# Performance work log

Hardware: AMD Instinct MI355X
Metric: run time of the kernel (lower is better)

## Reference

```python
import jax, jax.numpy as jnp
import numpy as np

N, D, E = 50000, 128, 800000
BN_EPS = 1e-5


def _gcn(x, W, b, row, col, val):
    # dropout with p=0.0 is identity; h = x @ W; out = adj @ h + b (COO SpMM)
    h = x @ W                                    # [N, d]
    msg = val[:, None] * h[col]                  # [E, d] gather + scale
    agg = jax.ops.segment_sum(msg, row, num_segments=x.shape[0])  # scatter-add
    return agg + b


def _predictor(x, W1, b1, gamma, beta, a, W2, b2):
    h = x @ W1 + b1
    mu = jnp.mean(h, axis=0)
    var = jnp.mean((h - mu) ** 2, axis=0)        # biased var (torch BN train mode)
    hn = (h - mu) / jnp.sqrt(var + BN_EPS) * gamma + beta
    hp = jnp.where(hn >= 0, hn, a * hn)          # PReLU, single shared alpha
    return hp @ W2 + b2


def _byol_loss(p, t):
    pn = p / jnp.linalg.norm(p, axis=-1, keepdims=True)
    tn = t / jnp.linalg.norm(t, axis=-1, keepdims=True)
    return 2.0 - 2.0 * jnp.sum(pn * tn, axis=-1)


def setup_inputs() -> dict:
    key = jax.random.key(0)
    ks = jax.random.split(key, 16)
    xavier = float(np.sqrt(6.0 / (D + D)))
    x = jax.random.normal(ks[0], (N, D), dtype=jnp.float32)
    perb = 0.05 * jax.random.normal(ks[1], (N, D), dtype=jnp.float32)
    edge_row = jax.random.randint(ks[2], (E,), 0, N, dtype=jnp.int32)
    edge_col = jax.random.randint(ks[3], (E,), 0, N, dtype=jnp.int32)
    edge_val = jax.random.uniform(ks[4], (E,), dtype=jnp.float32)
    W = jax.random.uniform(ks[5], (D, D), minval=-xavier, maxval=xavier, dtype=jnp.float32)
    b = jnp.zeros((D,), dtype=jnp.float32)
    # target encoder is a deepcopy at init; give it its own values to test the math
    Wt = jax.random.uniform(ks[6], (D, D), minval=-xavier, maxval=xavier, dtype=jnp.float32)
    bt = jnp.zeros((D,), dtype=jnp.float32)
    lin = float(1.0 / np.sqrt(D))
    W1 = jax.random.uniform(ks[7], (D, D), minval=-lin, maxval=lin, dtype=jnp.float32)
    b1 = jax.random.uniform(ks[8], (D,), minval=-lin, maxval=lin, dtype=jnp.float32)
    bn_gamma = jnp.ones((D,), dtype=jnp.float32)
    bn_beta = jnp.zeros((D,), dtype=jnp.float32)
    prelu_a = jnp.asarray(0.25, dtype=jnp.float32)
    W2 = jax.random.uniform(ks[9], (D, D), minval=-lin, maxval=lin, dtype=jnp.float32)
    b2 = jax.random.uniform(ks[10], (D,), minval=-lin, maxval=lin, dtype=jnp.float32)
    return dict(x=x, perb=perb, edge_row=edge_row, edge_col=edge_col, edge_val=edge_val,
                W=W, b=b, Wt=Wt, bt=bt, W1=W1, b1=b1, bn_gamma=bn_gamma,
                bn_beta=bn_beta, prelu_a=prelu_a, W2=W2, b2=b2)


def reference(x, perb, edge_row, edge_col, edge_val, W, b, Wt, bt,
              W1, b1, bn_gamma, bn_beta, prelu_a, W2, b2):
    x1 = x
    x2 = x + perb
    enc_x2 = _gcn(x2, W, b, edge_row, edge_col, edge_val)
    embed = x2 + enc_x2
    online_x = _gcn(x1, W, b, edge_row, edge_col, edge_val)
    online_y = enc_x2
    target_y = jax.lax.stop_gradient(_gcn(x1, Wt, bt, edge_row, edge_col, edge_val))
    target_x = jax.lax.stop_gradient(_gcn(x2, Wt, bt, edge_row, edge_col, edge_val))
    px = _predictor(online_x, W1, b1, bn_gamma, bn_beta, prelu_a, W2, b2)
    py = _predictor(online_y, W1, b1, bn_gamma, bn_beta, prelu_a, W2, b2)
    loss = jnp.mean(_byol_loss(px, target_x) + _byol_loss(py, target_y))
    return embed, loss
```

## Files before the change

### kernel.cpp

```cpp
#include <hip/hip_runtime.h>
#include <hip/hip_fp16.h>
#include <stdint.h>

typedef unsigned short u16;
typedef unsigned int u32;
typedef unsigned char u8;
typedef __attribute__((ext_vector_type(8))) short bf16x8;
typedef __attribute__((ext_vector_type(4))) short bf16x4;
typedef __attribute__((ext_vector_type(4))) float f32x4;

#define DD 128
#define CAP 64
#define STRA 136
#define STRCF 132
#define PSC 256.f
#define IPSC (1.f/256.f)

__device__ __forceinline__ float bflo(u32 u){ return __uint_as_float(u<<16); }
__device__ __forceinline__ float bfhi(u32 u){ return __uint_as_float(u & 0xffff0000u); }
__device__ __forceinline__ float bf2f(u16 u){ return __uint_as_float(((u32)u)<<16); }
__device__ __forceinline__ u16 f2bf(float f){
  u32 u = __float_as_uint(f);
  return (u16)((u + 0x7fffu + ((u>>16)&1u)) >> 16);
}

#define FMAXP(g, vv, vqv) do { \
    ax[0] += (vv)*bflo((g).x); ax[1] += (vv)*bfhi((g).x); \
    ax[2] += (vv)*bflo((g).y); ax[3] += (vv)*bfhi((g).y); \
    int d_ = (int)(g).z; \
    ap[0] += (vqv)*(float)(signed char)(d_); \
    ap[1] += (vqv)*(float)(signed char)(d_>>8); \
    ap[2] += (vqv)*(float)(signed char)(d_>>16); \
    ap[3] += (vqv)*(float)(d_>>24); } while(0)

__global__ __launch_bounds__(256) void kU_init(
    const float* __restrict__ x, const float* __restrict__ perb,
    const float* __restrict__ W, const float* __restrict__ Wt,
    const float* __restrict__ W1, const float* __restrict__ W2,
    u8* __restrict__ Tg, u16* __restrict__ Bswz,
    u16* __restrict__ W1swz, u16* __restrict__ W2swz,
    int* __restrict__ deg, float* __restrict__ stats,
    float* __restrict__ gbuf, int N)
{
  int f = blockIdx.x*256 + threadIdx.x;
  if (f < N) deg[f] = 0;
  if (f < 512) stats[f] = 0.f;
  if (f < 64) gbuf[f] = 0.f;
  if (f < 65536) {
    int idx = f;
    if (idx < 32768) {
      int j = idx & 7, lane = (idx>>3)&63, nt = (idx>>9)&15, kt = idx>>13;
      int k = kt*32 + (lane>>4)*8 + j, n = nt*16 + (lane&15);
      float v = (n < DD) ? W[k*DD + n] : Wt[k*DD + (n-DD)];
      Bswz[idx] = f2bf(v);
    } else {
      int t = idx - 32768;
      int which = t >> 14; t &= 16383;
      int j = t & 7, lane = (t>>3)&63, nt = (t>>9)&7, kt = (t>>12)&3;
      int k = kt*32 + (lane>>4)*8 + j, n = nt*16 + (lane&15);
      const float* __restrict__ src = which ? W2 : W1;
      u16* __restrict__ dst = which ? W2swz : W1swz;
      dst[t] = f2bf(src[k*DD + n]);
    }
  }
  if (f < N*32) {
    int r = f >> 5, hl = f & 31;
    float4 xa = *(const float4*)(x    + (size_t)r*DD + hl*4);
    float4 pa = *(const float4*)(perb + (size_t)r*DD + hl*4);
    u32 d0 = (u32)f2bf(xa.x) | ((u32)f2bf(xa.y) << 16);
    u32 d1 = (u32)f2bf(xa.z) | ((u32)f2bf(xa.w) << 16);
    int q0 = (int)rintf(pa.x*PSC); q0 = q0 < -127 ? -127 : (q0 > 127 ? 127 : q0);
    int q1 = (int)rintf(pa.y*PSC); q1 = q1 < -127 ? -127 : (q1 > 127 ? 127 : q1);
    int q2 = (int)rintf(pa.z*PSC); q2 = q2 < -127 ? -127 : (q2 > 127 ? 127 : q2);
    int q3 = (int)rintf(pa.w*PSC); q3 = q3 < -127 ? -127 : (q3 > 127 ? 127 : q3);
    u32 d2 = (u32)(q0 & 0xff) | ((u32)(q1 & 0xff) << 8)
           | ((u32)(q2 & 0xff) << 16) | ((u32)(q3 & 0xff) << 24);
    uint3 o; o.x = d0; o.y = d1; o.z = d2;
    *(uint3*)(Tg + (size_t)r*384 + hl*12) = o;
  }
}

__global__ __launch_bounds__(256) void k2_bucket(
    const int* __restrict__ row, const int* __restrict__ col,
    const float* __restrict__ val, int E, int* __restrict__ deg,
    u32* __restrict__ perm, int* __restrict__ ovfc, int* __restrict__ ovf)
{
  int e = blockIdx.x*256 + threadIdx.x;
  if (e >= E) return;
  int r = row[e];
  int slot = atomicAdd(&deg[r], 1);
  if (slot < CAP) {
    u32 pk = (u32)(col[e] & 0xffff)
           | ((u32)__half_as_ushort(__float2half(val[e])) << 16);
    perm[(size_t)r*CAP + slot] = pk;
  }
  else { int oi = atomicAdd(ovfc, 1); if (oi < 4096) ovf[oi] = e; }
}

__global__ __launch_bounds__(256) void k3_spmm(
    const u32* __restrict__ perm, const int* __restrict__ deg,
    const u8* __restrict__ Tg, u16* __restrict__ T2, int N)
{
  int row = blockIdx.x*4 + (threadIdx.x >> 6);
  int l = threadIdx.x & 63;
  if (row >= N) return;
  int dg = deg[row];
  dg = dg < 0 ? 0 : (dg > CAP ? CAP : dg);
  const int half = l >> 5, hl = l & 31;
  const int loff = hl * 12;
  float ax[4] = {0.f,0.f,0.f,0.f};
  float ap[4] = {0.f,0.f,0.f,0.f};
  for (int base = 0; base < dg; base += 64) {
    u32 pk = 0;
    if (base + l < dg) pk = perm[(size_t)row*CAP + base + l];
    int mm = dg - base; if (mm > 64) mm = 64;
    int kmax = (mm + 1) & ~1;
    int j = 0;
    for (; j + 8 <= kmax; j += 8) {
      u32 p0 = (u32)__shfl((int)pk, j + half);
      u32 p1 = (u32)__shfl((int)pk, j + 2 + half);
      u32 p2 = (u32)__shfl((int)pk, j + 4 + half);
      u32 p3 = (u32)__shfl((int)pk, j + 6 + half);
      int c0 = p0 & 0xffff; c0 = (c0 < N) ? c0 : 0;
      int c1 = p1 & 0xffff; c1 = (c1 < N) ? c1 : 0;
      int c2 = p2 & 0xffff; c2 = (c2 < N) ? c2 : 0;
      int c3 = p3 & 0xffff; c3 = (c3 < N) ? c3 : 0;
      float v0 = __half2float(__ushort_as_half((u16)(p0 >> 16)));
      float v1 = __half2float(__ushort_as_half((u16)(p1 >> 16)));
      float v2 = __half2float(__ushort_as_half((u16)(p2 >> 16)));
      float v3 = __half2float(__ushort_as_half((u16)(p3 >> 16)));
      uint3 g0 = *(const uint3*)(Tg + (size_t)c0*384 + loff);
      uint3 g1 = *(const uint3*)(Tg + (size_t)c1*384 + loff);
      uint3 g2 = *(const uint3*)(Tg + (size_t)c2*384 + loff);
      uint3 g3 = *(const uint3*)(Tg + (size_t)c3*384 + loff);
      float vq0 = v0*IPSC, vq1 = v1*IPSC, vq2 = v2*IPSC, vq3 = v3*IPSC;
      FMAXP(g0, v0, vq0); FMAXP(g1, v1, vq1);
      FMAXP(g2, v2, vq2); FMAXP(g3, v3, vq3);
    }
    for (; j < kmax; j += 2) {
      u32 p0 = (u32)__shfl((int)pk, j + half);
      int c0 = p0 & 0xffff; c0 = (c0 < N) ? c0 : 0;
      float v0 = __half2float(__ushort_as_half((u16)(p0 >> 16)));
      uint3 g0 = *(const uint3*)(Tg + (size_t)c0*384 + loff);
      float vq0 = v0*IPSC;
      FMAXP(g0, v0, vq0);
    }
  }
  #pragma unroll
  for (int i = 0; i < 4; ++i) {
    ax[i] += __shfl_xor(ax[i], 32);
    ap[i] += __shfl_xor(ap[i], 32);
  }
  bf16x4 ob;
  #pragma unroll
  for (int i = 0; i < 4; ++i) {
    float o = half ? (ax[i] + ap[i]) : ax[i];
    ob[i] = (short)f2bf(o);
  }
  *(bf16x4*)(T2 + (size_t)row*256 + half*128 + hl*4) = ob;
}

__global__ __launch_bounds__(256) void k3b_ovf(
    const int* __restrict__ rowI, const int* __restrict__ colI,
    const float* __restrict__ val, const int* __restrict__ ovfc,
    const int* __restrict__ ovf, const u8* __restrict__ Tg,
    u16* __restrict__ T2)
{
  int n = *ovfc; if (n > 4096) n = 4096;
  for (int i = 0; i < n; ++i) {
    int e = ovf[i];
    int r = rowI[e], c = colI[e];
    float v = val[e];
    int d = threadIdx.x;
    int dl = d & 127;
    const u8* tgc = Tg + (size_t)c*384 + (dl>>2)*12;
    float xv = bf2f(*(const u16*)(tgc + (dl&3)*2));
    float add = v * xv;
    if (d >= 128) {
      int qb = (int)(signed char)tgc[8 + (dl&3)];
      add = v * (xv + (float)qb * IPSC);
    }
    u16* p = &T2[(size_t)r*256 + d];
    *p = f2bf(bf2f(*p) + add);
  }
}

__global__ __launch_bounds__(256, 4) void k4_gemm(
    const u16* __restrict__ T2, const u16* __restrict__ Bswz,
    const u16* __restrict__ W1swz,
    const float* __restrict__ b, const float* __restrict__ bt,
    const float* __restrict__ b1, const u8* __restrict__ Tg,
    u16* __restrict__ AGGb, float* __restrict__ outE,
    u16* __restrict__ Px, u16* __restrict__ Py,
    float* __restrict__ partial, int N, int NB)
{
  __shared__ __align__(16) u16 As1[64*STRA];
  __shared__ __align__(16) u16 Ct[64*STRA];
  const int tid = threadIdx.x;
  const int r0 = blockIdx.x * 32;
  #pragma unroll
  for (int i = 0; i < 4; ++i) {
    int f = tid + 256*i;
    int row = f >> 4, c8 = f & 15;
    int r = r0 + (row & 31);
    bf16x8 ch = {0,0,0,0,0,0,0,0};
    if (r < N) ch = *(const bf16x8*)(T2 + (size_t)r*256 + (row>>5)*128 + c8*8);
    *(bf16x8*)&As1[row*STRA + c8*8] = ch;
  }
  __syncthreads();
  const int w = tid >> 6, l = tid & 63;
  const int m = l & 15, q = l >> 4;
  const int arow = w*16 + m;
  f32x4 acc[8];
  #pragma unroll
  for (int nt = 0; nt < 8; ++nt) acc[nt] = (f32x4){0.f,0.f,0.f,0.f};
  #pragma unroll
  for (int kt = 0; kt < 4; ++kt) {
    bf16x8 af = *(const bf16x8*)&As1[arow*STRA + kt*32 + q*8];
    #pragma unroll
    for (int nt = 0; nt < 8; ++nt) {
      bf16x8 bfr = *(const bf16x8*)(Bswz + ((size_t)(kt*16 + 8 + nt)*64 + l)*8);
      acc[nt] = __builtin_amdgcn_mfma_f32_16x16x32_bf16(af, bfr, acc[nt], 0, 0, 0);
    }
  }
  #pragma unroll
  for (int nt = 0; nt < 8; ++nt) {
    float bv = bt[nt*16 + m];
    #pragma unroll
    for (int i = 0; i < 4; ++i)
      Ct[(w*16 + q*4 + i)*STRA + nt*16 + m] = f2bf(acc[nt][i] + bv);
  }
  __syncthreads();
  {
    const int ar = tid >> 2, p = tid & 3;
    const int src = r0 + (ar & 31);
    if (src < N) {
      u16* dp = AGGb + (size_t)src*256 + (ar>>5)*128 + p*32;
      const u16* sp = &Ct[ar*STRA + p*32];
      #pragma unroll
      for (int i = 0; i < 4; ++i)
        *(bf16x8*)(dp + i*8) = *(const bf16x8*)(sp + i*8);
    }
  }
  __syncthreads();
  #pragma unroll
  for (int nt = 0; nt < 8; ++nt) acc[nt] = (f32x4){0.f,0.f,0.f,0.f};
  #pragma unroll
  for (int kt = 0; kt < 4; ++kt) {
    bf16x8 af = *(const bf16x8*)&As1[arow*STRA + kt*32 + q*8];
    #pragma unroll
    for (int nt = 0; nt < 8; ++nt) {
      bf16x8 bfr = *(const bf16x8*)(Bswz + ((size_t)(kt*16 + nt)*64 + l)*8);
      acc[nt] = __builtin_amdgcn_mfma_f32_16x16x32_bf16(af, bfr, acc[nt], 0, 0, 0);
    }
  }
  #pragma unroll
  for (int nt = 0; nt < 8; ++nt) {
    float bv = b[nt*16 + m];
    #pragma unroll
    for (int i = 0; i < 4; ++i)
      Ct[(w*16 + q*4 + i)*STRA + nt*16 + m] = f2bf(acc[nt][i] + bv);
  }
  __syncthreads();
  #pragma unroll
  for (int i = 0; i < 2; ++i) {
    int f = tid + 256*i;
    int rr = f >> 4, c8 = f & 15;
    int src = r0 + rr;
    if (src < N) {
      const u16* cp = &Ct[(32+rr)*STRA + c8*8];
      const u8* tg = Tg + (size_t)src*384 + c8*24;
      uint3 ga = *(const uint3*)tg;
      uint3 gb = *(const uint3*)(tg + 12);
      int da = (int)ga.z, db = (int)gb.z;
      float4 e0, e1;
      e0.x = bflo(ga.x) + IPSC*(float)(signed char)(da)     + bf2f(cp[0]);
      e0.y = bfhi(ga.x) + IPSC*(float)(signed char)(da>>8)  + bf2f(cp[1]);
      e0.z = bflo(ga.y) + IPSC*(float)(signed char)(da>>16) + bf2f(cp[2]);
      e0.w = bfhi(ga.y) + IPSC*(float)(da>>24)              + bf2f(cp[3]);
      e1.x = bflo(gb.x) + IPSC*(float)(signed char)(db)     + bf2f(cp[4]);
      e1.y = bfhi(gb.x) + IPSC*(float)(signed char)(db>>8)  + bf2f(cp[5]);
      e1.z = bflo(gb.y) + IPSC*(float)(signed char)(db>>16) + bf2f(cp[6]);
      e1.w = bfhi(gb.y) + IPSC*(float)(db>>24)              + bf2f(cp[7]);
      float* er = outE + (size_t)src*DD + c8*8;
      *(float4*)er = e0;
      *(float4*)(er+4) = e1;
    }
  }
  #pragma unroll
  for (int nt = 0; nt < 8; ++nt) acc[nt] = (f32x4){0.f,0.f,0.f,0.f};
  #pragma unroll
  for (int kt = 0; kt < 4; ++kt) {
    bf16x8 af = *(const bf16x8*)&Ct[arow*STRA + kt*32 + q*8];
    #pragma unroll
    for (int nt = 0; nt < 8; ++nt) {
      bf16x8 bfr = *(const bf16x8*)(W1swz + ((size_t)(kt*8+nt)*64 + l)*8);
      acc[nt] = __builtin_amdgcn_mfma_f32_16x16x32_bf16(af, bfr, acc[nt], 0, 0, 0);
    }
  }
  float* red = (float*)As1;
  #pragma unroll
  for (int nt = 0; nt < 8; ++nt) {
    float bv = b1[nt*16 + m];
    float sum = 0.f, sq = 0.f;
    #pragma unroll
    for (int i = 0; i < 4; ++i) {
      int src = r0 + ((w*16 + q*4 + i) & 31);
      if (src < N) acc[nt][i] += bv; else acc[nt][i] = 0.f;
      sum += acc[nt][i]; sq += acc[nt][i]*acc[nt][i];
    }
    sum += __shfl_xor(sum, 16); sum += __shfl_xor(sum, 32);
    sq  += __shfl_xor(sq, 16);  sq  += __shfl_xor(sq, 32);
    if (l < 16) {
      red[      w*128 + nt*16 + l] = sum;
      red[512 + w*128 + nt*16 + l] = sq;
    }
  }
  __syncthreads();
  {
    int type = tid >> 7, col = tid & 127;
    float v0 = red[type*512 +   0 + col] + red[type*512 + 128 + col];
    float v1 = red[type*512 + 256 + col] + red[type*512 + 384 + col];
    partial[((size_t)0*NB + blockIdx.x)*256 + tid] = v0;
    partial[((size_t)1*NB + blockIdx.x)*256 + tid] = v1;
  }
  #pragma unroll
  for (int nt = 0; nt < 8; ++nt)
    #pragma unroll
    for (int i = 0; i < 4; ++i)
      Ct[(w*16 + q*4 + i)*STRA + nt*16 + m] = f2bf(acc[nt][i]);
  __syncthreads();
  {
    const int ar = tid >> 2, p = tid & 3;
    const int src = r0 + (ar & 31);
    if (src < N) {
      const u16* sp = &Ct[ar*STRA + p*32];
      u16* dp = ((ar >> 5) ? Py : Px) + (size_t)src*DD + p*32;
      #pragma unroll
      for (int i = 0; i < 4; ++i)
        *(bf16x8*)(dp + i*8) = *(const bf16x8*)(sp + i*8);
    }
  }
}

__global__ __launch_bounds__(256) void k5b_stats(
    const float* __restrict__ partial, float* __restrict__ stats, int nb)
{
  int seg = blockIdx.y, chunk = blockIdx.x, t = threadIdx.x;
  int per = (nb + gridDim.x - 1) / gridDim.x;
  int lo = chunk*per, hi = lo+per; if (hi > nb) hi = nb;
  float s = 0.f;
  const float* p = partial + (size_t)seg*nb*256;
  for (int i = lo; i < hi; ++i) s += p[(size_t)i*256 + t];
  atomicAdd(&stats[seg*256 + t], s);
}

__global__ __launch_bounds__(256) void k6_gemm_loss(
    const u16* __restrict__ Px, const u16* __restrict__ Py,
    const u16* __restrict__ AGGb, const float* __restrict__ stats,
    const float* __restrict__ gamma, const float* __restrict__ beta,
    const float* __restrict__ aP, const u16* __restrict__ W2swz,
    const float* __restrict__ b2, float* __restrict__ gloss, int N)
{
  __shared__ __align__(16) float Cs[64*STRCF];
  u16* As = (u16*)Cs;
  __shared__ float s1s[128], s2s[128];
  __shared__ float gred[4];
  const int tid = threadIdx.x;
  const int seg = blockIdx.y;
  const u16* __restrict__ P = seg ? Py : Px;
  const int toff = seg ? 0 : 128;
  const float invN = 1.f / (float)N;
  if (tid < 128) {
    float mu = stats[seg*256 + tid] * invN;
    float var = stats[seg*256 + 128 + tid] * invN - mu*mu;
    float rstd = rsqrtf(var + 1e-5f);
    float s1 = rstd * gamma[tid];
    s1s[tid] = s1;
    s2s[tid] = beta[tid] - mu*s1;
  }
  const float alpha = aP[0];
  const int r0 = blockIdx.x * 64;
  __syncthreads();
  #pragma unroll
  for (int i = 0; i < 4; ++i) {
    int f = tid + 256*i;
    int row = f >> 4, c8 = f & 15;
    int r = r0 + row;
    bf16x8 ch = {0,0,0,0,0,0,0,0};
    if (r < N) ch = *(const bf16x8*)(P + (size_t)r*DD + c8*8);
    bf16x8 a;
    #pragma unroll
    for (int t2 = 0; t2 < 8; ++t2) {
      int colc = c8*8 + t2;
      float hv = bf2f((u16)ch[t2]);
      float hn = hv*s1s[colc] + s2s[colc];
      hn = hn >= 0.f ? hn : alpha*hn;
      a[t2] = (short)f2bf(hn);
    }
    *(bf16x8*)&As[row*STRA + c8*8] = a;
  }
  __syncthreads();
  const int w = tid >> 6, l = tid & 63;
  const int m = l & 15, q = l >> 4;
  f32x4 acc[8];
  #pragma unroll
  for (int nt = 0; nt < 8; ++nt) acc[nt] = (f32x4){0.f,0.f,0.f,0.f};
  const int arow = w*16 + m;
  #pragma unroll
  for (int kt = 0; kt < 4; ++kt) {
    bf16x8 af = *(const bf16x8*)&As[arow*STRA + kt*32 + q*8];
    #pragma unroll
    for (int nt = 0; nt < 8; ++nt) {
      bf16x8 bfr = *(const bf16x8*)(W2swz + ((size_t)(kt*8+nt)*64 + l)*8);
      acc[nt] = __builtin_amdgcn_mfma_f32_16x16x32_bf16(af, bfr, acc[nt], 0, 0, 0);
    }
  }
  __syncthreads();
  #pragma unroll
  for (int nt = 0; nt < 8; ++nt) {
    float bv = b2[nt*16 + m];
    #pragma unroll
    for (int i = 0; i < 4; ++i)
      Cs[(w*16 + q*4 + i)*STRCF + nt*16 + m] = acc[nt][i] + bv;
  }
  __syncthreads();
  {
    const int rt = tid >> 2, qq = tid & 3;
    const int r = r0 + rt;
    float pp = 0.f, tt = 0.f, pt = 0.f;
    if (r < N) {
      const float* prow = &Cs[rt*STRCF + qq*32];
      const u16* trow = AGGb + (size_t)r*256 + toff + qq*32;
      #pragma unroll
      for (int i = 0; i < 4; ++i) {
        float4 pa = *(const float4*)(prow + i*8);
        float4 pb = *(const float4*)(prow + i*8 + 4);
        uint4 twv = *(const uint4*)(trow + i*8);
        float t0=bflo(twv.x), t1=bfhi(twv.x), t2=bflo(twv.y), t3=bfhi(twv.y);
        float t4=bflo(twv.z), t5=bfhi(twv.z), t6=bflo(twv.w), t7=bfhi(twv.w);
        pp += pa.x*pa.x + pa.y*pa.y + pa.z*pa.z + pa.w*pa.w
            + pb.x*pb.x + pb.y*pb.y + pb.z*pb.z + pb.w*pb.w;
        tt += t0*t0 + t1*t1 + t2*t2 + t3*t3 + t4*t4 + t5*t5 + t6*t6 + t7*t7;
        pt += pa.x*t0 + pa.y*t1 + pa.z*t2 + pa.w*t3
            + pb.x*t4 + pb.y*t5 + pb.z*t6 + pb.w*t7;
      }
    }
    pp += __shfl_xor(pp, 1); pp += __shfl_xor(pp, 2);
    tt += __shfl_xor(tt, 1); tt += __shfl_xor(tt, 2);
    pt += __shfl_xor(pt, 1); pt += __shfl_xor(pt, 2);
    float lsum = (r < N) ? (2.f - 2.f * pt * rsqrtf(pp * tt)) : 0.f;
    lsum += __shfl_xor(lsum, 4);  lsum += __shfl_xor(lsum, 8);
    lsum += __shfl_xor(lsum, 16); lsum += __shfl_xor(lsum, 32);
    if (l == 0) gred[w] = lsum;
  }
  __syncthreads();
  if (tid == 0) atomicAdd(gloss, gred[0]+gred[1]+gred[2]+gred[3]);
}

__global__ void k7_loss(const float* __restrict__ gloss, float* __restrict__ out, int N, int total)
{
  out[total] = gloss[0] / (float)N;
}

extern "C" void kernel_launch(void* const* d_in, const int* in_sizes, int n_in,
                              void* d_out, int out_size, void* d_ws, size_t ws_size,
                              hipStream_t stream)
{
  const float* x    = (const float*)d_in[0];
  const float* perb = (const float*)d_in[1];
  const int*   erow = (const int*)d_in[2];
  const int*   ecol = (const int*)d_in[3];
  const float* eval_= (const float*)d_in[4];
  const float* W    = (const float*)d_in[5];
  const float* b    = (const float*)d_in[6];
  const float* Wt   = (const float*)d_in[7];
  const float* bt   = (const float*)d_in[8];
  const float* W1   = (const float*)d_in[9];
  const float* b1   = (const float*)d_in[10];
  const float* gam  = (const float*)d_in[11];
  const float* bet  = (const float*)d_in[12];
  const float* aP   = (const float*)d_in[13];
  const float* W2   = (const float*)d_in[14];
  const float* b2   = (const float*)d_in[15];
  const int N = in_sizes[0] / DD;
  const int E = in_sizes[2];
  const int NB4 = (N + 31)/32;
  const int NB5 = (N + 63)/64;

  char* ws = (char*)d_ws;
  size_t off = 0;
  auto alloc = [&](size_t bytes) -> void* {
    void* p = ws + off;
    off += (bytes + 255) & ~(size_t)255;
    return p;
  };
  u16*   AGGb = (u16*)  alloc((size_t)N*256*sizeof(u16));
  u8*    Tg   = (u8*)   alloc((size_t)N*384);
  u16*   T2   = (u16*)  alloc((size_t)N*256*sizeof(u16));
  u16*   Px   = (u16*)  alloc((size_t)N*DD*sizeof(u16));
  u16*   Py   = (u16*)  alloc((size_t)N*DD*sizeof(u16));
  int*   deg  = (int*)  alloc((size_t)N*sizeof(int));
  float* stats= (float*)alloc(512*sizeof(float));
  float* gloss= (float*)alloc(256);
  int*   ovfc = (int*)((char*)gloss + 64);
  u32*   perm = (u32*)  alloc((size_t)N*CAP*sizeof(u32));
  int*   ovf  = (int*)  alloc(4096*sizeof(int));
  u16*   Bswz = (u16*)  alloc(32768*sizeof(u16));
  u16*   W1swz= (u16*)  alloc(16384*sizeof(u16));
  u16*   W2swz= (u16*)  alloc(16384*sizeof(u16));
  float* partial = (float*)alloc((size_t)2*NB4*256*sizeof(float));
  if (ws_size < off) return;

  kU_init<<<(N*32 + 255)/256, 256, 0, stream>>>(x, perb, W, Wt, W1, W2,
                                                Tg, Bswz, W1swz, W2swz,
                                                deg, stats, gloss, N);
  k2_bucket<<<(E + 255)/256, 256, 0, stream>>>(erow, ecol, eval_, E, deg, perm, ovfc, ovf);
  k3_spmm<<<(N + 3)/4, 256, 0, stream>>>(perm, deg, Tg, T2, N);
  k3b_ovf<<<1, 256, 0, stream>>>(erow, ecol, eval_, ovfc, ovf, Tg, T2);
  k4_gemm<<<NB4, 256, 0, stream>>>(T2, Bswz, W1swz, b, bt, b1, Tg,
                                   AGGb, (float*)d_out, Px, Py, partial, N, NB4);
  k5b_stats<<<dim3(16, 2), 256, 0, stream>>>(partial, stats, NB4);
  k6_gemm_loss<<<dim3(NB5, 2), 256, 0, stream>>>(Px, Py, AGGb, stats, gam, bet, aP,
                                                 W2swz, b2, gloss, N);
  k7_loss<<<1, 1, 0, stream>>>(gloss, (float*)d_out, N, N*DD);
}
```

Before: 313.8 us.

## Split MFMA tiles by output columns per wave so B fragments load once

The warp tiling of the 64x128 block GEMMs changes from each wave owning 16 rows and all 128 columns to each wave owning 32 columns and all 64 rows. Each wave now loads only its 8 B-fragments from global memory into registers once, instead of streaming all 32 per k-step, and re-reads A fragments from LDS instead. BN partial-sum reduction is restructured to match the new layout. The cost is more LDS A-fragment reads and a different accumulator pattern.

New measurement: 299.8 us. 1.05x faster.

```diff
diff --git a/kernel.cpp b/kernel.cpp
--- a/kernel.cpp
+++ b/kernel.cpp
@@ -210,25 +210,35 @@
   __syncthreads();
   const int w = tid >> 6, l = tid & 63;
   const int m = l & 15, q = l >> 4;
-  const int arow = w*16 + m;
-  f32x4 acc[8];
-  #pragma unroll
-  for (int nt = 0; nt < 8; ++nt) acc[nt] = (f32x4){0.f,0.f,0.f,0.f};
-  #pragma unroll
-  for (int kt = 0; kt < 4; ++kt) {
-    bf16x8 af = *(const bf16x8*)&As1[arow*STRA + kt*32 + q*8];
-    #pragma unroll
-    for (int nt = 0; nt < 8; ++nt) {
-      bf16x8 bfr = *(const bf16x8*)(Bswz + ((size_t)(kt*16 + 8 + nt)*64 + l)*8);
-      acc[nt] = __builtin_amdgcn_mfma_f32_16x16x32_bf16(af, bfr, acc[nt], 0, 0, 0);
-    }
-  }
-  #pragma unroll
-  for (int nt = 0; nt < 8; ++nt) {
-    float bv = bt[nt*16 + m];
-    #pragma unroll
-    for (int i = 0; i < 4; ++i)
-      Ct[(w*16 + q*4 + i)*STRA + nt*16 + m] = f2bf(acc[nt][i] + bv);
+  const int cbase = w*32 + m;
+  f32x4 acc[4][2];
+  bf16x8 bfrag[2][4];
+  #pragma unroll
+  for (int ntl = 0; ntl < 2; ++ntl)
+    #pragma unroll
+    for (int kt = 0; kt < 4; ++kt)
+      bfrag[ntl][kt] = *(const bf16x8*)(Bswz + ((size_t)(kt*16 + 8 + w*2 + ntl)*64 + l)*8);
+  #pragma unroll
+  for (int rt = 0; rt < 4; ++rt) {
+    acc[rt][0] = (f32x4){0.f,0.f,0.f,0.f};
+    acc[rt][1] = (f32x4){0.f,0.f,0.f,0.f};
+  }
+  #pragma unroll
+  for (int kt = 0; kt < 4; ++kt)
+    #pragma unroll
+    for (int rt = 0; rt < 4; ++rt) {
+      bf16x8 af = *(const bf16x8*)&As1[(rt*16 + m)*STRA + kt*32 + q*8];
+      acc[rt][0] = __builtin_amdgcn_mfma_f32_16x16x32_bf16(af, bfrag[0][kt], acc[rt][0], 0, 0, 0);
+      acc[rt][1] = __builtin_amdgcn_mfma_f32_16x16x32_bf16(af, bfrag[1][kt], acc[rt][1], 0, 0, 0);
+    }
+  #pragma unroll
+  for (int ntl = 0; ntl < 2; ++ntl) {
+    float bv = bt[cbase + ntl*16];
+    #pragma unroll
+    for (int rt = 0; rt < 4; ++rt)
+      #pragma unroll
+      for (int i = 0; i < 4; ++i)
+        Ct[(rt*16 + q*4 + i)*STRA + cbase + ntl*16] = f2bf(acc[rt][ntl][i] + bv);
   }
   __syncthreads();
   {
@@ -244,22 +254,31 @@
   }
   __syncthreads();
   #pragma unroll
-  for (int nt = 0; nt < 8; ++nt) acc[nt] = (f32x4){0.f,0.f,0.f,0.f};
-  #pragma unroll
-  for (int kt = 0; kt < 4; ++kt) {
-    bf16x8 af = *(const bf16x8*)&As1[arow*STRA + kt*32 + q*8];
-    #pragma unroll
-    for (int nt = 0; nt < 8; ++nt) {
-      bf16x8 bfr = *(const bf16x8*)(Bswz + ((size_t)(kt*16 + nt)*64 + l)*8);
-      acc[nt] = __builtin_amdgcn_mfma_f32_16x16x32_bf16(af, bfr, acc[nt], 0, 0, 0);
-    }
-  }
-  #pragma unroll
-  for (int nt = 0; nt < 8; ++nt) {
-    float bv = b[nt*16 + m];
-    #pragma unroll
-    for (int i = 0; i < 4; ++i)
-      Ct[(w*16 + q*4 + i)*STRA + nt*16 + m] = f2bf(acc[nt][i] + bv);
+  for (int ntl = 0; ntl < 2; ++ntl)
+    #pragma unroll
+    for (int kt = 0; kt < 4; ++kt)
+      bfrag[ntl][kt] = *(const bf16x8*)(Bswz + ((size_t)(kt*16 + w*2 + ntl)*64 + l)*8);
+  #pragma unroll
+  for (int rt = 0; rt < 4; ++rt) {
+    acc[rt][0] = (f32x4){0.f,0.f,0.f,0.f};
+    acc[rt][1] = (f32x4){0.f,0.f,0.f,0.f};
+  }
+  #pragma unroll
+  for (int kt = 0; kt < 4; ++kt)
+    #pragma unroll
+    for (int rt = 0; rt < 4; ++rt) {
+      bf16x8 af = *(const bf16x8*)&As1[(rt*16 + m)*STRA + kt*32 + q*8];
+      acc[rt][0] = __builtin_amdgcn_mfma_f32_16x16x32_bf16(af, bfrag[0][kt], acc[rt][0], 0, 0, 0);
+      acc[rt][1] = __builtin_amdgcn_mfma_f32_16x16x32_bf16(af, bfrag[1][kt], acc[rt][1], 0, 0, 0);
+    }
+  #pragma unroll
+  for (int ntl = 0; ntl < 2; ++ntl) {
+    float bv = b[cbase + ntl*16];
+    #pragma unroll
+    for (int rt = 0; rt < 4; ++rt)
+      #pragma unroll
+      for (int i = 0; i < 4; ++i)
+        Ct[(rt*16 + q*4 + i)*STRA + cbase + ntl*16] = f2bf(acc[rt][ntl][i] + bv);
   }
   __syncthreads();
   #pragma unroll
@@ -288,47 +307,64 @@
     }
   }
   #pragma unroll
-  for (int nt = 0; nt < 8; ++nt) acc[nt] = (f32x4){0.f,0.f,0.f,0.f};
-  #pragma unroll
-  for (int kt = 0; kt < 4; ++kt) {
-    bf16x8 af = *(const bf16x8*)&Ct[arow*STRA + kt*32 + q*8];
-    #pragma unroll
-    for (int nt = 0; nt < 8; ++nt) {
-      bf16x8 bfr = *(const bf16x8*)(W1swz + ((size_t)(kt*8+nt)*64 + l)*8);
-      acc[nt] = __builtin_amdgcn_mfma_f32_16x16x32_bf16(af, bfr, acc[nt], 0, 0, 0);
-    }
-  }
+  for (int ntl = 0; ntl < 2; ++ntl)
+    #pragma unroll
+    for (int kt = 0; kt < 4; ++kt)
+      bfrag[ntl][kt] = *(const bf16x8*)(W1swz + ((size_t)(kt*8 + w*2 + ntl)*64 + l)*8);
+  #pragma unroll
+  for (int rt = 0; rt < 4; ++rt) {
+    acc[rt][0] = (f32x4){0.f,0.f,0.f,0.f};
+    acc[rt][1] = (f32x4){0.f,0.f,0.f,0.f};
+  }
+  #pragma unroll
+  for (int kt = 0; kt < 4; ++kt)
+    #pragma unroll
+    for (int rt = 0; rt < 4; ++rt) {
+      bf16x8 af = *(const bf16x8*)&Ct[(rt*16 + m)*STRA + kt*32 + q*8];
+      acc[rt][0] = __builtin_amdgcn_mfma_f32_16x16x32_bf16(af, bfrag[0][kt], acc[rt][0], 0, 0, 0);
+      acc[rt][1] = __builtin_amdgcn_mfma_f32_16x16x32_bf16(af, bfrag[1][kt], acc[rt][1], 0, 0, 0);
+    }
   float* red = (float*)As1;
   #pragma unroll
-  for (int nt = 0; nt < 8; ++nt) {
-    float bv = b1[nt*16 + m];
-    float sum = 0.f, sq = 0.f;
-    #pragma unroll
-    for (int i = 0; i < 4; ++i) {
-      int src = r0 + ((w*16 + q*4 + i) & 31);
-      if (src < N) acc[nt][i] += bv; else acc[nt][i] = 0.f;
-      sum += acc[nt][i]; sq += acc[nt][i]*acc[nt][i];
-    }
-    sum += __shfl_xor(sum, 16); sum += __shfl_xor(sum, 32);
-    sq  += __shfl_xor(sq, 16);  sq  += __shfl_xor(sq, 32);
+  for (int ntl = 0; ntl < 2; ++ntl) {
+    float bv = b1[cbase + ntl*16];
+    float s0 = 0.f, s1 = 0.f, q0 = 0.f, q1 = 0.f;
+    #pragma unroll
+    for (int rt = 0; rt < 4; ++rt)
+      #pragma unroll
+      for (int i = 0; i < 4; ++i) {
+        int src = r0 + (((rt*16 + q*4 + i)) & 31);
+        float v = (src < N) ? (acc[rt][ntl][i] + bv) : 0.f;
+        acc[rt][ntl][i] = v;
+        if (rt < 2) { s0 += v; q0 += v*v; } else { s1 += v; q1 += v*v; }
+      }
+    s0 += __shfl_xor(s0, 16); s0 += __shfl_xor(s0, 32);
+    s1 += __shfl_xor(s1, 16); s1 += __shfl_xor(s1, 32);
+    q0 += __shfl_xor(q0, 16); q0 += __shfl_xor(q0, 32);
+    q1 += __shfl_xor(q1, 16); q1 += __shfl_xor(q1, 32);
     if (l < 16) {
-      red[      w*128 + nt*16 + l] = sum;
-      red[512 + w*128 + nt*16 + l] = sq;
+      int c = cbase + ntl*16;
+      red[          c] = s0;
+      red[128     + c] = s1;
+      red[256     + c] = q0;
+      red[256+128 + c] = q1;
     }
   }
   __syncthreads();
   {
     int type = tid >> 7, col = tid & 127;
-    float v0 = red[type*512 +   0 + col] + red[type*512 + 128 + col];
-    float v1 = red[type*512 + 256 + col] + red[type*512 + 384 + col];
+    float v0 = red[type*256 + col];
+    float v1 = red[type*256 + 128 + col];
     partial[((size_t)0*NB + blockIdx.x)*256 + tid] = v0;
     partial[((size_t)1*NB + blockIdx.x)*256 + tid] = v1;
   }
   #pragma unroll
-  for (int nt = 0; nt < 8; ++nt)
-    #pragma unroll
-    for (int i = 0; i < 4; ++i)
-      Ct[(w*16 + q*4 + i)*STRA + nt*16 + m] = f2bf(acc[nt][i]);
+  for (int ntl = 0; ntl < 2; ++ntl)
+    #pragma unroll
+    for (int rt = 0; rt < 4; ++rt)
+      #pragma unroll
+      for (int i = 0; i < 4; ++i)
+        Ct[(rt*16 + q*4 + i)*STRA + cbase + ntl*16] = f2bf(acc[rt][ntl][i]);
   __syncthreads();
   {
     const int ar = tid >> 2, p = tid & 3;
@@ -403,26 +439,36 @@
   __syncthreads();
   const int w = tid >> 6, l = tid & 63;
   const int m = l & 15, q = l >> 4;
-  f32x4 acc[8];
-  #pragma unroll
-  for (int nt = 0; nt < 8; ++nt) acc[nt] = (f32x4){0.f,0.f,0.f,0.f};
-  const int arow = w*16 + m;
-  #pragma unroll
-  for (int kt = 0; kt < 4; ++kt) {
-    bf16x8 af = *(const bf16x8*)&As[arow*STRA + kt*32 + q*8];
-    #pragma unroll
-    for (int nt = 0; nt < 8; ++nt) {
-      bf16x8 bfr = *(const bf16x8*)(W2swz + ((size_t)(kt*8+nt)*64 + l)*8);
-      acc[nt] = __builtin_amdgcn_mfma_f32_16x16x32_bf16(af, bfr, acc[nt], 0, 0, 0);
-    }
-  }
-  __syncthreads();
-  #pragma unroll
-  for (int nt = 0; nt < 8; ++nt) {
-    float bv = b2[nt*16 + m];
-    #pragma unroll
-    for (int i = 0; i < 4; ++i)
-      Cs[(w*16 + q*4 + i)*STRCF + nt*16 + m] = acc[nt][i] + bv;
+  const int cbase = w*32 + m;
+  f32x4 acc[4][2];
+  bf16x8 bfrag[2][4];
+  #pragma unroll
+  for (int ntl = 0; ntl < 2; ++ntl)
+    #pragma unroll
+    for (int kt = 0; kt < 4; ++kt)
+      bfrag[ntl][kt] = *(const bf16x8*)(W2swz + ((size_t)(kt*8 + w*2 + ntl)*64 + l)*8);
+  #pragma unroll
+  for (int rt = 0; rt < 4; ++rt) {
+    acc[rt][0] = (f32x4){0.f,0.f,0.f,0.f};
+    acc[rt][1] = (f32x4){0.f,0.f,0.f,0.f};
+  }
+  #pragma unroll
+  for (int kt = 0; kt < 4; ++kt)
+    #pragma unroll
+    for (int rt = 0; rt < 4; ++rt) {
+      bf16x8 af = *(const bf16x8*)&As[(rt*16 + m)*STRA + kt*32 + q*8];
+      acc[rt][0] = __builtin_amdgcn_mfma_f32_16x16x32_bf16(af, bfrag[0][kt], acc[rt][0], 0, 0, 0);
+      acc[rt][1] = __builtin_amdgcn_mfma_f32_16x16x32_bf16(af, bfrag[1][kt], acc[rt][1], 0, 0, 0);
+    }
+  __syncthreads();
+  #pragma unroll
+  for (int ntl = 0; ntl < 2; ++ntl) {
+    float bv = b2[cbase + ntl*16];
+    #pragma unroll
+    for (int rt = 0; rt < 4; ++rt)
+      #pragma unroll
+      for (int i = 0; i < 4; ++i)
+        Cs[(rt*16 + q*4 + i)*STRCF + cbase + ntl*16] = acc[rt][ntl][i] + bv;
   }
   __syncthreads();
   {
```
